# Kernel optimization log

Measured on AMD Instinct MI355X. Metric: run time of the kernel, lower is better.

The kernel has to match this reference:

```python
import jax, jax.numpy as jnp
import numpy as np

RES = 256
XYZ_MIN, XYZ_MAX = -1.0, 1.0
STEPSIZE = 1.0
NEAR, FAR, BG = 0.2, 3.0, 1.0
ALPHA_INIT = 0.01
ACT_SHIFT = float(np.log(1.0 / (1.0 - ALPHA_INIT) - 1.0))
VOXEL = (XYZ_MAX - XYZ_MIN) / RES  # (prod(extent)/R^3)^(1/3) = 2/256
N_SAMPLES = int(np.linalg.norm(np.array([RES + 1] * 3, dtype=np.float64)) / STEPSIZE) + 1  # 446
N_RAYS = 4096
LATENT, NFEAT, RGB_LAT = 64, 32, 15
MULTIRES = 6


def _dense(key, din, dout):
    kw, kb = jax.random.split(key)
    return (jax.random.normal(kw, (din, dout), jnp.float32) / np.float32(np.sqrt(din)),
            jax.random.normal(kb, (dout,), jnp.float32) * 0.01)


def setup_inputs():
    ks = jax.random.split(jax.random.key(0), 16)
    rays_o = jax.random.normal(ks[0], (N_RAYS, 3), jnp.float32) * 1.5
    rays_d = jax.random.normal(ks[1], (N_RAYS, 3), jnp.float32)
    viewdirs = rays_d / jnp.linalg.norm(rays_d, axis=-1, keepdims=True)
    mW1, mb1 = _dense(ks[2], 4, 128)
    mW2, mb2 = _dense(ks[3], 128, 128)
    mW3, mb3 = _dense(ks[4], 128, NFEAT)
    pW1, pb1 = _dense(ks[5], LATENT, 64)
    pW2, pb2 = _dense(ks[6], 64, 64)
    pW3, pb3 = _dense(ks[7], 64, 1 + RGB_LAT)
    emb_dim = 3 + 3 * 2 * MULTIRES  # 39
    dW1, db1 = _dense(ks[8], RGB_LAT + emb_dim, 64)
    dW2, db2 = _dense(ks[9], 64, 64)
    dW3, db3 = _dense(ks[10], 64, 64)
    dW4, db4 = _dense(ks[11], 64, 3)
    return dict(
        rays_o=rays_o, rays_d=rays_d, viewdirs=viewdirs,
        mapping_grid=jax.random.normal(ks[12], (4, RES, RES, RES), jnp.float32) * 0.1,
        feature_vectors=jax.random.normal(ks[13], (NFEAT, LATENT), jnp.float32) * 0.1,
        mW1=mW1, mb1=mb1, mW2=mW2, mb2=mb2, mW3=mW3, mb3=mb3,
        pW1=pW1, pb1=pb1, pW2=pW2, pb2=pb2, pW3=pW3, pb3=pb3,
        dW1=dW1, db1=db1, dW2=dW2, db2=db2, dW3=dW3, db3=db3, dW4=dW4, db4=db4)


def _trilinear(grid, pts):
    # grid: [C,R,R,R]; pts: [...,3] world coords; matches F.grid_sample(align_corners=True)
    # after the flip(-1) in the original (x indexes dim0 of the volume).
    g = jnp.transpose(grid, (1, 2, 3, 0))  # [R,R,R,C]
    u = (pts - XYZ_MIN) / (XYZ_MAX - XYZ_MIN)
    idx = jnp.clip(u * (RES - 1), 0.0, RES - 1.0)
    i0 = jnp.clip(jnp.floor(idx).astype(jnp.int32), 0, RES - 2)
    f = idx - i0.astype(idx.dtype)
    x0, y0, z0 = i0[..., 0], i0[..., 1], i0[..., 2]
    x1, y1, z1 = x0 + 1, y0 + 1, z0 + 1
    fx, fy, fz = f[..., 0:1], f[..., 1:2], f[..., 2:3]
    c000, c001 = g[x0, y0, z0], g[x0, y0, z1]
    c010, c011 = g[x0, y1, z0], g[x0, y1, z1]
    c100, c101 = g[x1, y0, z0], g[x1, y0, z1]
    c110, c111 = g[x1, y1, z0], g[x1, y1, z1]
    c00 = c000 * (1 - fz) + c001 * fz
    c01 = c010 * (1 - fz) + c011 * fz
    c10 = c100 * (1 - fz) + c101 * fz
    c11 = c110 * (1 - fz) + c111 * fz
    c0 = c00 * (1 - fy) + c01 * fy
    c1 = c10 * (1 - fy) + c11 * fy
    return c0 * (1 - fx) + c1 * fx


def _mlp3(x, W1, b1, W2, b2, W3, b3):
    h = jax.nn.relu(x @ W1 + b1)
    h = jax.nn.relu(h @ W2 + b2)
    return h @ W3 + b3


def _dir_embed(v):
    # NeRF positional encoding: [v, sin(2^i v), cos(2^i v)] for i in [0, MULTIRES)
    freqs = 2.0 ** jnp.arange(MULTIRES, dtype=v.dtype)  # [L]
    ang = v[..., None, :] * freqs[:, None]              # [N,L,3]
    sc = jnp.concatenate([jnp.sin(ang), jnp.cos(ang)], axis=-1)  # [N,L,6]
    return jnp.concatenate([v, sc.reshape(v.shape[0], 2 * 3 * MULTIRES)], axis=-1)  # [N,39]


def reference(rays_o, rays_d, viewdirs, mapping_grid, feature_vectors,
              mW1, mb1, mW2, mb2, mW3, mb3,
              pW1, pb1, pW2, pb2, pW3, pb3,
              dW1, db1, dW2, db2, dW3, db3, dW4, db4):
    # --- ray sampling (is_train=False, no jitter) ---
    vec = jnp.where(rays_d == 0, 1e-6, rays_d)
    rate_a = (XYZ_MAX - rays_o) / vec
    rate_b = (XYZ_MIN - rays_o) / vec
    t_min = jnp.clip(jnp.minimum(rate_a, rate_b).max(-1), NEAR, FAR)
    t_max = jnp.clip(jnp.maximum(rate_a, rate_b).min(-1), NEAR, FAR)
    step = STEPSIZE * VOXEL * jnp.arange(N_SAMPLES, dtype=rays_o.dtype)  # [S]
    interpx = t_min[:, None] + step[None, :] / jnp.linalg.norm(rays_d, axis=-1, keepdims=True)
    ray_pts = rays_o[:, None, :] + rays_d[:, None, :] * interpx[..., None]  # [N,S,3]
    valid = ~((t_max <= t_min)[:, None]
              | jnp.any((ray_pts < XYZ_MIN) | (ray_pts > XYZ_MAX), axis=-1))  # [N,S]

    # --- latent extraction: grid sample -> attention over feature bank ---
    mp = _trilinear(mapping_grid, ray_pts)                                  # [N,S,4]
    attn = jax.nn.softmax(_mlp3(mp, mW1, mb1, mW2, mb2, mW3, mb3), axis=-1)  # [N,S,F]
    latent = attn @ feature_vectors                                          # [N,S,latent]

    # --- positional MLP -> density + rgb latent (masked entries zeroed as in torch) ---
    pos = _mlp3(latent, pW1, pb1, pW2, pb2, pW3, pb3)  # [N,S,1+rgb_lat]
    alpha = jnp.where(valid,
                      1.0 - jnp.exp(-jax.nn.softplus(pos[..., 0] + ACT_SHIFT) * STEPSIZE),
                      0.0)
    rgb_latent = jnp.where(valid[..., None], pos[..., 1:], 0.0)

    # --- alpha compositing weights ---
    alphainv_cum = jnp.concatenate(
        [jnp.ones_like(alpha[..., :1]),
         jnp.cumprod(jnp.clip(1.0 - alpha, 1e-10, None), axis=-1)], axis=-1)  # [N,S+1]
    weights = alpha * alphainv_cum[..., :-1]

    # --- directional MLP -> rgb ---
    emb = _dir_embed(viewdirs)                                               # [N,39]
    emb = jnp.broadcast_to(emb[:, None, :], (alpha.shape[0], alpha.shape[1], emb.shape[-1]))
    rgb_feat = jnp.concatenate([rgb_latent, emb], axis=-1)                   # [N,S,54]
    h = jax.nn.relu(rgb_feat @ dW1 + db1)
    h = jax.nn.relu(h @ dW2 + db2)
    h = jax.nn.relu(h @ dW3 + db3)
    raw_rgb = h @ dW4 + db4
    rgb = jnp.where(valid[..., None], jax.nn.sigmoid(raw_rgb[..., :3]), 0.0)

    rgb_marched = jnp.einsum('ns,nsc->nc', weights, rgb) + alphainv_cum[..., -1:] * BG
    return rgb_marched
```

## Files before the change

kernel.cpp:

```cpp
#include <hip/hip_runtime.h>
#include <math.h>

#define ACT_SHIFT -4.5951198501345889f
#define SB 96
#define NSLOTMAX (4096*446)
#define MLP_BLOCKS 1024

typedef _Float16 f16;
typedef f16 f16x8 __attribute__((ext_vector_type(8)));
typedef f16 f16x4 __attribute__((ext_vector_type(4)));
typedef f16 f16x2 __attribute__((ext_vector_type(2)));
typedef float f32x4 __attribute__((ext_vector_type(4)));

#define OFF_CNT  0
#define OFF_RAYI 256
#define OFF_RAYF (OFF_RAYI + 4096*16)
#define OFF_EMBW (OFF_RAYF + 4096*8)
#define OFF_WTS  (OFF_EMBW + 4096*64*4)
#define OFF_SLOT (OFF_WTS + 94208)
#define OFF_WS4H (OFF_SLOT + NSLOTMAX*4)

#define W_MW1 0
#define W_MW2 4096
#define W_MW3 20480
#define W_FV  24576
#define W_P1  26624
#define W_P2  30720
#define W_P3  34816
#define W_D1  35840
#define W_D2  37888
#define W_D3  41984
#define W_D4  46080
#define W_TOT 47104

static __device__ __forceinline__ unsigned short f2h(float x) {
  f16 h = (f16)x; return *(unsigned short*)&h;
}
static __device__ __forceinline__ float h2f(unsigned short u) {
  return (float)(*(f16*)&u);
}

static __device__ __forceinline__ void bar_lds() {
  asm volatile("s_waitcnt lgkmcnt(0)" ::: "memory");
  __builtin_amdgcn_s_barrier();
}

static __device__ __forceinline__ void sample_point(
    float ox, float oy, float oz, float dx, float dy, float dz,
    float tmin, float nrm, int s, float& px, float& py, float& pz) {
  float ix = tmin + (0.0078125f * (float)s) / nrm;
  px = ox + dx * ix; py = oy + dy * ix; pz = oz + dz * ix;
}
static __device__ __forceinline__ int in_box(float px, float py, float pz) {
  return !(px < -1.f || px > 1.f || py < -1.f || py > 1.f ||
           pz < -1.f || pz > 1.f);
}

static __device__ __forceinline__ bool ray_setup(
    const float* rays_o, const float* rays_d, int r,
    float& ox, float& oy, float& oz, float& dx, float& dy, float& dz,
    float& tmin, float& nrm) {
  ox = rays_o[r*3+0]; oy = rays_o[r*3+1]; oz = rays_o[r*3+2];
  dx = rays_d[r*3+0]; dy = rays_d[r*3+1]; dz = rays_d[r*3+2];
  const float vx = (dx == 0.0f) ? 1e-6f : dx;
  const float vy = (dy == 0.0f) ? 1e-6f : dy;
  const float vz = (dz == 0.0f) ? 1e-6f : dz;
  const float rax = ( 1.0f - ox) / vx, rbx = (-1.0f - ox) / vx;
  const float ray_ = ( 1.0f - oy) / vy, rby = (-1.0f - oy) / vy;
  const float raz = ( 1.0f - oz) / vz, rbz = (-1.0f - oz) / vz;
  tmin = fmaxf(fmaxf(fminf(rax,rbx), fminf(ray_,rby)), fminf(raz,rbz));
  tmin = fminf(fmaxf(tmin, 0.2f), 3.0f);
  float tmax = fminf(fminf(fmaxf(rax,rbx), fmaxf(ray_,rby)), fmaxf(raz,rbz));
  tmax = fminf(fmaxf(tmax, 0.2f), 3.0f);
  nrm = sqrtf(dx*dx + dy*dy + dz*dz);
  return tmax <= tmin;
}

extern "C" __global__ void __launch_bounds__(256)
k_setup(const float* __restrict__ rays_o, const float* __restrict__ rays_d,
        int* __restrict__ cnt, int4* __restrict__ rayi,
        float2* __restrict__ rayf) {
  int r = blockIdx.x * 256 + threadIdx.x;
  if (r >= 4096) return;
  float ox,oy,oz,dx,dy,dz,tmin,nrm;
  bool miss = ray_setup(rays_o, rays_d, r, ox,oy,oz,dx,dy,dz, tmin, nrm);
  rayf[r] = make_float2(tmin, nrm);
  if (miss) { rayi[r] = make_int4(0,0,0,0); return; }

  float lo = -1e30f, hi = 1e30f;
  float o3[3] = {ox,oy,oz}, d3[3] = {dx,dy,dz};
#pragma unroll
  for (int c = 0; c < 3; ++c) {
    float o = o3[c], d = d3[c];
    if (d == 0.0f) {
      if (o < -1.f || o > 1.f) { lo = 1e30f; hi = -1e30f; }
    } else {
      float t1 = (-1.f - o) / d, t2 = (1.f - o) / d;
      lo = fmaxf(lo, fminf(t1, t2));
      hi = fminf(hi, fmaxf(t1, t2));
    }
  }
  float k = 0.0078125f / nrm;
  float sf = (lo - tmin) / k - 1.0f;
  float lf = (hi - tmin) / k + 1.0f;
  int first = (int)ceilf (fmaxf(0.f,  fminf(445.f, sf)));
  int last  = (int)floorf(fmaxf(-1.f, fminf(445.f, lf)));
  int n_s = (lf >= sf && last >= first) ? (last - first + 1) : 0;
  int base = 0;
  if (n_s > 0) base = atomicAdd(cnt, n_s);
  rayi[r] = make_int4(base, first, n_s, 0);
}

extern "C" __global__ void __launch_bounds__(64)
k_fill(const int4* __restrict__ rayi, int* __restrict__ slot_map) {
  int r = blockIdx.x;
  int4 ri = rayi[r];
  for (int i = threadIdx.x; i < ri.z; i += 64)
    slot_map[ri.x + i] = (r << 9) | (ri.y + i);
}

extern "C" __global__ void __launch_bounds__(256)
k_embw(const float* __restrict__ viewdirs, const float* __restrict__ dW1,
       const float* __restrict__ db1, float* __restrict__ embW) {
  int idx = blockIdx.x * 256 + threadIdx.x;
  if (idx >= 4096*64) return;
  int ray = idx >> 6, o = idx & 63;
  float v0 = viewdirs[ray*3+0], v1 = viewdirs[ray*3+1], v2 = viewdirs[ray*3+2];
  float acc = db1[o];
  acc = fmaf(v0, dW1[15*64+o], acc);
  acc = fmaf(v1, dW1[16*64+o], acc);
  acc = fmaf(v2, dW1[17*64+o], acc);
#pragma unroll
  for (int fr = 0; fr < 6; ++fr) {
    float f = (float)(1 << fr);
    int rb = 18 + fr*6;
    acc = fmaf(sinf(v0*f), dW1[(rb+0)*64+o], acc);
    acc = fmaf(sinf(v1*f), dW1[(rb+1)*64+o], acc);
    acc = fmaf(sinf(v2*f), dW1[(rb+2)*64+o], acc);
    acc = fmaf(cosf(v0*f), dW1[(rb+3)*64+o], acc);
    acc = fmaf(cosf(v1*f), dW1[(rb+4)*64+o], acc);
    acc = fmaf(cosf(v2*f), dW1[(rb+5)*64+o], acc);
  }
  embW[idx] = acc;
}

extern "C" __global__ void __launch_bounds__(256)
k_pack(const float* __restrict__ mW1, const float* __restrict__ mW2,
       const float* __restrict__ mW3, const float* __restrict__ fv,
       const float* __restrict__ pW1, const float* __restrict__ pW2,
       const float* __restrict__ pW3, const float* __restrict__ dW1,
       const float* __restrict__ dW2, const float* __restrict__ dW3,
       const float* __restrict__ dW4, f16* __restrict__ wts) {
  int i = blockIdx.x * 256 + threadIdx.x;
  if (i >= W_TOT) return;
  float v = 0.f; int l, o, k;
  if (i < W_MW2)        { l=i-W_MW1; o=l>>5; k=l&31;  if (k<4)  v = mW1[k*128+o]; }
  else if (i < W_MW3)   { l=i-W_MW2; o=l>>7; k=l&127; v = mW2[k*128+o]; }
  else if (i < W_FV)    { l=i-W_MW3; o=l>>7; k=l&127; v = mW3[k*32+o]; }
  else if (i < W_P1)    { l=i-W_FV;  o=l>>5; k=l&31;  v = fv[k*64+o]; }
  else if (i < W_P2)    { l=i-W_P1;  o=l>>6; k=l&63;  v = pW1[k*64+o]; }
  else if (i < W_P3)    { l=i-W_P2;  o=l>>6; k=l&63;  v = pW2[k*64+o]; }
  else if (i < W_D1)    { l=i-W_P3;  o=l>>6; k=l&63;  v = pW3[k*16+o]; }
  else if (i < W_D2)    { l=i-W_D1;  o=l>>5; k=l&31;  if (k>=1 && k<16) v = dW1[(k-1)*64+o]; }
  else if (i < W_D3)    { l=i-W_D2;  o=l>>6; k=l&63;  v = dW2[k*64+o]; }
  else if (i < W_D4)    { l=i-W_D3;  o=l>>6; k=l&63;  v = dW3[k*64+o]; }
  else                  { l=i-W_D4;  o=l>>6; k=l&63;  if (o<3)  v = dW4[k*3+o]; }
  wts[i] = (f16)v;
}

template<int KP, int NP, bool RELU, int BMODE, int NW>
__device__ __forceinline__ void layer_mm(
    const f16* __restrict__ Wt, const float* __restrict__ bias,
    const float* __restrict__ embW, const int* sinfo,
    const f16* inb, f16* outb, int wave, int lane,
    int blockbase, unsigned short* ws4h, float& alpha_reg, int& pk_reg) {
  constexpr int ST = SB/16, MT = NP/16, NT = MT*ST, TPW = (NT+NW-1)/NW, KS = KP/32;
  const int c = lane & 15, g = lane >> 4;
  f16x8 Af[KS];
  f32x4 b4 = {0.f,0.f,0.f,0.f};
  int prev_dt = -1;
#pragma unroll
  for (int ti = 0; ti < TPW; ++ti) {
    int t = wave * TPW + ti;
    if (t >= NT) break;
    int dt = t / ST, st = t % ST;
    if (dt != prev_dt) {
      prev_dt = dt;
      const f16* wp = Wt + (size_t)(dt*16 + c) * KP + g*8;
#pragma unroll
      for (int ks = 0; ks < KS; ++ks)
        Af[ks] = *(const f16x8*)(wp + ks*32);
      if (BMODE == 1 || BMODE == 3 || BMODE == 4)
        b4 = *(const f32x4*)(bias + dt*16 + g*4);
    }
    const int row = st*16 + c;
    f32x4 acc = {0.f,0.f,0.f,0.f};
#pragma unroll
    for (int ks = 0; ks < KS; ++ks) {
      int off = (row*256 + (ks*32 + g*8)*2) ^ ((row & 7) << 4);
      f16x8 Bf = *(const f16x8*)((const char*)inb + off);
      acc = __builtin_amdgcn_mfma_f32_16x16x32_f16(Af[ks], Bf, acc, 0, 0, 0);
    }
    if (BMODE == 2) {
      int pk = sinfo[row];
      int ry = (pk < 0) ? 0 : (pk >> 1);
      b4 = *(const f32x4*)(embW + ry*64 + dt*16 + g*4);
    }
    float v0 = acc[0]+b4[0], v1 = acc[1]+b4[1];
    float v2 = acc[2]+b4[2], v3 = acc[3]+b4[3];
    if (BMODE <= 2) {
      if (RELU) {
        v0 = fmaxf(v0,0.f); v1 = fmaxf(v1,0.f);
        v2 = fmaxf(v2,0.f); v3 = fmaxf(v3,0.f);
      }
      f16x4 o = {(f16)v0,(f16)v1,(f16)v2,(f16)v3};
      int off = (row*256 + (dt*16 + g*4)*2) ^ ((row & 7) << 4);
      *(f16x4*)((char*)outb + off) = o;
    } else if (BMODE == 3) {
      pk_reg = sinfo[row];
      if (g == 0) {
        float a = 0.f;
        if (pk_reg >= 0 && (pk_reg & 1)) {
          float x = v0 + ACT_SHIFT;
          float sp = fmaxf(x, 0.f) + log1pf(expf(-fabsf(x)));
          a = 1.f - expf(-sp);
        }
        alpha_reg = a;
        v0 = 0.f;
      }
      f16x4 o = {(f16)v0,(f16)v1,(f16)v2,(f16)v3};
      int off = (row*256 + (g*4)*2) ^ ((row & 7) << 4);
      *(f16x4*)((char*)outb + off) = o;
    } else {
      if (g == 0 && pk_reg >= 0) {
        bool val = (pk_reg & 1) != 0;
        ushort4 u;
        u.x = f2h(alpha_reg);
        u.y = f2h(val ? (1.f/(1.f+expf(-v0))) : 0.f);
        u.z = f2h(val ? (1.f/(1.f+expf(-v1))) : 0.f);
        u.w = f2h(val ? (1.f/(1.f+expf(-v2))) : 0.f);
        *(ushort4*)(ws4h + (size_t)(blockbase + row)*4) = u;
      }
    }
  }
}

struct Pf {
  float v[8];
  float fx, fy, fz;
  int pk;
};

static __device__ __forceinline__ void pf_issue(
    int slot, int total, int c,
    const int* __restrict__ slot_map, const float2* __restrict__ rayf,
    const float* __restrict__ rays_o, const float* __restrict__ rays_d,
    const float* __restrict__ grid, Pf& P) {
  if (slot >= total) {
    P.pk = -2; P.fx = P.fy = P.fz = 0.f;
#pragma unroll
    for (int i = 0; i < 8; ++i) P.v[i] = 0.f;
    return;
  }
  int mi = slot_map[slot];
  int ray = mi >> 9, s = mi & 511;
  float2 tf = rayf[ray];
  float ox = rays_o[ray*3+0], oy = rays_o[ray*3+1], oz = rays_o[ray*3+2];
  float dx = rays_d[ray*3+0], dy = rays_d[ray*3+1], dz = rays_d[ray*3+2];
  float px, py, pz;
  sample_point(ox,oy,oz,dx,dy,dz, tf.x, tf.y, s, px,py,pz);
  P.pk = ray*2 + in_box(px,py,pz);
  float ixf = fminf(fmaxf((px + 1.f) * 0.5f * 255.f, 0.f), 255.f);
  float iyf = fminf(fmaxf((py + 1.f) * 0.5f * 255.f, 0.f), 255.f);
  float izf = fminf(fmaxf((pz + 1.f) * 0.5f * 255.f, 0.f), 255.f);
  int x0 = min((int)ixf, 254), y0 = min((int)iyf, 254), z0 = min((int)izf, 254);
  P.fx = ixf - (float)x0; P.fy = iyf - (float)y0; P.fz = izf - (float)z0;
  const float* gc = grid + (size_t)c * 16777216u;
  int bx0 = x0 << 16, bx1 = bx0 + 65536;
  int by0 = y0 << 8,  by1 = by0 + 256;
  P.v[0] = gc[bx0+by0+z0]; P.v[1] = gc[bx0+by0+z0+1];
  P.v[2] = gc[bx0+by1+z0]; P.v[3] = gc[bx0+by1+z0+1];
  P.v[4] = gc[bx1+by0+z0]; P.v[5] = gc[bx1+by0+z0+1];
  P.v[6] = gc[bx1+by1+z0]; P.v[7] = gc[bx1+by1+z0+1];
}

extern "C" __global__ void __launch_bounds__(512)
k_mlp(const float* __restrict__ rays_o, const float* __restrict__ rays_d,
      const float* __restrict__ grid, const int* __restrict__ slot_map,
      const float2* __restrict__ rayf, const float* __restrict__ embW,
      const f16* __restrict__ wts, const int* __restrict__ cnt,
      const float* __restrict__ mb1, const float* __restrict__ mb2,
      const float* __restrict__ mb3, const float* __restrict__ pb1,
      const float* __restrict__ pb2, const float* __restrict__ pb3,
      const float* __restrict__ db2, const float* __restrict__ db3,
      const float* __restrict__ db4, unsigned short* __restrict__ ws4h) {
  const int total = *cnt;
  const int nch = (total + SB - 1) / SB;
  const int tid = threadIdx.x;
  const int wave = tid >> 6, lane = tid & 63;
  const int sl = tid >> 2, ch = tid & 3;

  __shared__ __align__(16) f16 X[SB*128];
  __shared__ __align__(16) f16 Y[SB*128];
  __shared__ int sinfo[SB];

  Pf P;
  if (tid < SB*4)
    pf_issue(blockIdx.x * SB + sl, total, ch, slot_map, rayf, rays_o, rays_d,
             grid, P);

  for (int chunk = blockIdx.x; chunk < nch; chunk += gridDim.x) {
    const int blockbase = chunk * SB;
    float alpha_reg = 0.f; int pk_reg = -2;

    if (tid < SB*4) {
      float c00 = P.v[0]*(1.f-P.fz) + P.v[1]*P.fz;
      float c01 = P.v[2]*(1.f-P.fz) + P.v[3]*P.fz;
      float c10 = P.v[4]*(1.f-P.fz) + P.v[5]*P.fz;
      float c11 = P.v[6]*(1.f-P.fz) + P.v[7]*P.fz;
      float c0v = c00*(1.f-P.fy) + c01*P.fy;
      float c1v = c10*(1.f-P.fy) + c11*P.fy;
      float mv  = c0v*(1.f-P.fx) + c1v*P.fx;
      if (ch == 0) sinfo[sl] = P.pk;
      int off = (sl*256 + ch*2) ^ ((sl & 7) << 4);
      *(f16*)((char*)X + off) = (f16)mv;
    }
    for (int idx = tid; idx < SB*14; idx += 512) {
      int row = idx / 14, dim = 4 + (idx % 14)*2;
      int off = (row*256 + dim*2) ^ ((row & 7) << 4);
      f16x2 z = {(f16)0.f, (f16)0.f};
      *(f16x2*)((char*)X + off) = z;
    }
    if (tid < SB*4)
      pf_issue((chunk + gridDim.x) * SB + sl, total, ch, slot_map, rayf,
               rays_o, rays_d, grid, P);
    bar_lds();

    layer_mm<32,128,true,1,8>(wts+W_MW1, mb1, nullptr, sinfo, X, Y, wave, lane, blockbase, ws4h, alpha_reg, pk_reg);
    bar_lds();
    layer_mm<128,128,true,1,8>(wts+W_MW2, mb2, nullptr, sinfo, Y, X, wave, lane, blockbase, ws4h, alpha_reg, pk_reg);
    bar_lds();
    layer_mm<128,32,false,1,8>(wts+W_MW3, mb3, nullptr, sinfo, X, Y, wave, lane, blockbase, ws4h, alpha_reg, pk_reg);
    bar_lds();

    if (tid < SB) {
      int row = tid;
      float v[32];
#pragma unroll
      for (int p = 0; p < 16; ++p) {
        int off = (row*256 + p*4) ^ ((row & 7) << 4);
        f16x2 two = *(const f16x2*)((const char*)Y + off);
        v[2*p] = (float)two[0]; v[2*p+1] = (float)two[1];
      }
      float m = -1e30f;
#pragma unroll
      for (int i = 0; i < 32; ++i) m = fmaxf(m, v[i]);
      float sum = 0.f;
#pragma unroll
      for (int i = 0; i < 32; ++i) { v[i] = expf(v[i] - m); sum += v[i]; }
      float inv = 1.f / sum;
#pragma unroll
      for (int p = 0; p < 16; ++p) {
        int off = (row*256 + p*4) ^ ((row & 7) << 4);
        f16x2 two = {(f16)(v[2*p]*inv), (f16)(v[2*p+1]*inv)};
        *(f16x2*)((char*)Y + off) = two;
      }
    }
    bar_lds();

    layer_mm<32,64,false,0,8>(wts+W_FV, nullptr, nullptr, sinfo, Y, X, wave, lane, blockbase, ws4h, alpha_reg, pk_reg);
    bar_lds();
    layer_mm<64,64,true,1,8>(wts+W_P1, pb1, nullptr, sinfo, X, Y, wave, lane, blockbase, ws4h, alpha_reg, pk_reg);
    bar_lds();
    layer_mm<64,64,true,1,8>(wts+W_P2, pb2, nullptr, sinfo, Y, X, wave, lane, blockbase, ws4h, alpha_reg, pk_reg);
    bar_lds();
    layer_mm<64,16,false,3,8>(wts+W_P3, pb3, nullptr, sinfo, X, Y, wave, lane, blockbase, ws4h, alpha_reg, pk_reg);
    bar_lds();
    layer_mm<32,64,true,2,8>(wts+W_D1, nullptr, embW, sinfo, Y, X, wave, lane, blockbase, ws4h, alpha_reg, pk_reg);
    bar_lds();
    layer_mm<64,64,true,1,8>(wts+W_D2, db2, nullptr, sinfo, X, Y, wave, lane, blockbase, ws4h, alpha_reg, pk_reg);
    bar_lds();
    layer_mm<64,64,true,1,8>(wts+W_D3, db3, nullptr, sinfo, Y, X, wave, lane, blockbase, ws4h, alpha_reg, pk_reg);
    bar_lds();
    layer_mm<64,16,false,4,8>(wts+W_D4, db4, nullptr, sinfo, X, Y, wave, lane, blockbase, ws4h, alpha_reg, pk_reg);
    bar_lds();
  }
}

extern "C" __global__ void __launch_bounds__(256)
k_scan(const ushort4* __restrict__ ws4h, const int4* __restrict__ rayi,
       float* __restrict__ out) {
  const int wid = (blockIdx.x * 256 + threadIdx.x) >> 6;
  const int ln  = threadIdx.x & 63;
  if (wid >= 4096) return;
  int4 ri = rayi[wid];
  int base = ri.x, n_s = ri.z;

  float T = 1.0f, ar = 0.f, ag = 0.f, ab = 0.f;
  int nc = (n_s + 63) >> 6;
  for (int cck = 0; cck < nc; ++cck) {
    int j = cck*64 + ln;
    float a = 0.f, rr = 0.f, gg = 0.f, bb = 0.f;
    if (j < n_s) {
      ushort4 u = ws4h[(size_t)base + j];
      a = h2f(u.x); rr = h2f(u.y); gg = h2f(u.z); bb = h2f(u.w);
    }
    float p = fmaxf(1.0f - a, 1e-10f);
#pragma unroll
    for (int off = 1; off < 64; off <<= 1) {
      float o = __shfl_up(p, off);
      if (ln >= off) p *= o;
    }
    float pe = __shfl_up(p, 1);
    if (ln == 0) pe = 1.0f;
    float wgt = a * T * pe;
    ar = fmaf(wgt, rr, ar);
    ag = fmaf(wgt, gg, ag);
    ab = fmaf(wgt, bb, ab);
    T *= __shfl(p, 63);
  }
#pragma unroll
  for (int off = 32; off; off >>= 1) {
    ar += __shfl_down(ar, off);
    ag += __shfl_down(ag, off);
    ab += __shfl_down(ab, off);
  }
  if (ln == 0) {
    out[wid*3+0] = ar + T;
    out[wid*3+1] = ag + T;
    out[wid*3+2] = ab + T;
  }
}

extern "C" void kernel_launch(void* const* d_in, const int* in_sizes, int n_in,
                              void* d_out, int out_size, void* d_ws, size_t ws_size,
                              hipStream_t stream) {
  const float* rays_o   = (const float*)d_in[0];
  const float* rays_d   = (const float*)d_in[1];
  const float* viewdirs = (const float*)d_in[2];
  const float* grid     = (const float*)d_in[3];
  const float* fv       = (const float*)d_in[4];
  const float* mW1 = (const float*)d_in[5];  const float* mb1 = (const float*)d_in[6];
  const float* mW2 = (const float*)d_in[7];  const float* mb2 = (const float*)d_in[8];
  const float* mW3 = (const float*)d_in[9];  const float* mb3 = (const float*)d_in[10];
  const float* pW1 = (const float*)d_in[11]; const float* pb1 = (const float*)d_in[12];
  const float* pW2 = (const float*)d_in[13]; const float* pb2 = (const float*)d_in[14];
  const float* pW3 = (const float*)d_in[15]; const float* pb3 = (const float*)d_in[16];
  const float* dW1 = (const float*)d_in[17]; const float* db1 = (const float*)d_in[18];
  const float* dW2 = (const float*)d_in[19]; const float* db2 = (const float*)d_in[20];
  const float* dW3 = (const float*)d_in[21]; const float* db3 = (const float*)d_in[22];
  const float* dW4 = (const float*)d_in[23]; const float* db4 = (const float*)d_in[24];
  float* out = (float*)d_out;

  char* ws = (char*)d_ws;
  int*     cnt      = (int*)(ws + OFF_CNT);
  int4*    rayi     = (int4*)(ws + OFF_RAYI);
  float2*  rayf     = (float2*)(ws + OFF_RAYF);
  float*   embW     = (float*)(ws + OFF_EMBW);
  f16*     wts      = (f16*)(ws + OFF_WTS);
  int*     slot_map = (int*)(ws + OFF_SLOT);
  unsigned short* ws4h = (unsigned short*)(ws + OFF_WS4H);

  hipMemsetAsync(cnt, 0, 4, stream);
  k_setup<<<16, 256, 0, stream>>>(rays_o, rays_d, cnt, rayi, rayf);
  k_fill<<<4096, 64, 0, stream>>>(rayi, slot_map);
  k_embw<<<1024, 256, 0, stream>>>(viewdirs, dW1, db1, embW);
  k_pack<<<(W_TOT+255)/256, 256, 0, stream>>>(mW1, mW2, mW3, fv, pW1, pW2, pW3,
                                              dW1, dW2, dW3, dW4, wts);
  k_mlp<<<MLP_BLOCKS, 512, 0, stream>>>(rays_o, rays_d, grid, slot_map, rayf,
                                        embW, wts, cnt, mb1, mb2, mb3,
                                        pb1, pb2, pb3, db2, db3, db4, ws4h);
  k_scan<<<1024, 256, 0, stream>>>((const ushort4*)ws4h, rayi, out);
}
```

Before: 105.4 us.

## Switch MLP to 32x32 MFMA with register-resident weights and dynamic chunk queue

Rewrites the fused MLP kernel to use 32x32x16 MFMA tiles on 128-sample chunks, keeping most layer weights resident in registers across chunks instead of reloading them per tile. Chunks are handed out through an atomic work queue with 256 persistent blocks rather than a fixed grid stride. The softmax is computed in registers straight from the MFMA accumulators. The fill, embedding and weight-pack kernels are merged into one auxiliary launch, and biases are packed into a padded buffer. The intent is to cut weight reload traffic, per-tile overhead and launch count, at the cost of much higher register pressure and lower occupancy.

```diff
diff --git a/kernel.cpp b/kernel.cpp
--- a/kernel.cpp
+++ b/kernel.cpp
@@ -2,36 +2,36 @@
 #include <math.h>
 
 #define ACT_SHIFT -4.5951198501345889f
-#define SB 96
+#define SB 128
 #define NSLOTMAX (4096*446)
-#define MLP_BLOCKS 1024
 
 typedef _Float16 f16;
 typedef f16 f16x8 __attribute__((ext_vector_type(8)));
 typedef f16 f16x4 __attribute__((ext_vector_type(4)));
-typedef f16 f16x2 __attribute__((ext_vector_type(2)));
 typedef float f32x4 __attribute__((ext_vector_type(4)));
+typedef float f32x16 __attribute__((ext_vector_type(16)));
 
 #define OFF_CNT  0
 #define OFF_RAYI 256
 #define OFF_RAYF (OFF_RAYI + 4096*16)
 #define OFF_EMBW (OFF_RAYF + 4096*8)
 #define OFF_WTS  (OFF_EMBW + 4096*64*4)
-#define OFF_SLOT (OFF_WTS + 94208)
+#define OFF_BIAS (OFF_WTS + 92160)
+#define OFF_SLOT (OFF_BIAS + 8192)
 #define OFF_WS4H (OFF_SLOT + NSLOTMAX*4)
 
 #define W_MW1 0
-#define W_MW2 4096
-#define W_MW3 20480
-#define W_FV  24576
-#define W_P1  26624
-#define W_P2  30720
-#define W_P3  34816
-#define W_D1  35840
-#define W_D2  37888
-#define W_D3  41984
-#define W_D4  46080
-#define W_TOT 47104
+#define W_MW2 2048
+#define W_MW3 18432
+#define W_FV  22528
+#define W_P1  24576
+#define W_P2  28672
+#define W_P3  32768
+#define W_D1  34816
+#define W_D2  35840
+#define W_D3  39936
+#define W_D4  44032
+#define W_TOT 46080
 
 static __device__ __forceinline__ unsigned short f2h(float x) {
   f16 h = (f16)x; return *(unsigned short*)&h;
@@ -111,137 +111,132 @@
   rayi[r] = make_int4(base, first, n_s, 0);
 }
 
-extern "C" __global__ void __launch_bounds__(64)
-k_fill(const int4* __restrict__ rayi, int* __restrict__ slot_map) {
-  int r = blockIdx.x;
-  int4 ri = rayi[r];
-  for (int i = threadIdx.x; i < ri.z; i += 64)
-    slot_map[ri.x + i] = (r << 9) | (ri.y + i);
-}
-
 extern "C" __global__ void __launch_bounds__(256)
-k_embw(const float* __restrict__ viewdirs, const float* __restrict__ dW1,
-       const float* __restrict__ db1, float* __restrict__ embW) {
-  int idx = blockIdx.x * 256 + threadIdx.x;
-  if (idx >= 4096*64) return;
-  int ray = idx >> 6, o = idx & 63;
-  float v0 = viewdirs[ray*3+0], v1 = viewdirs[ray*3+1], v2 = viewdirs[ray*3+2];
-  float acc = db1[o];
-  acc = fmaf(v0, dW1[15*64+o], acc);
-  acc = fmaf(v1, dW1[16*64+o], acc);
-  acc = fmaf(v2, dW1[17*64+o], acc);
-#pragma unroll
-  for (int fr = 0; fr < 6; ++fr) {
-    float f = (float)(1 << fr);
-    int rb = 18 + fr*6;
-    acc = fmaf(sinf(v0*f), dW1[(rb+0)*64+o], acc);
-    acc = fmaf(sinf(v1*f), dW1[(rb+1)*64+o], acc);
-    acc = fmaf(sinf(v2*f), dW1[(rb+2)*64+o], acc);
-    acc = fmaf(cosf(v0*f), dW1[(rb+3)*64+o], acc);
-    acc = fmaf(cosf(v1*f), dW1[(rb+4)*64+o], acc);
-    acc = fmaf(cosf(v2*f), dW1[(rb+5)*64+o], acc);
-  }
-  embW[idx] = acc;
-}
-
-extern "C" __global__ void __launch_bounds__(256)
-k_pack(const float* __restrict__ mW1, const float* __restrict__ mW2,
-       const float* __restrict__ mW3, const float* __restrict__ fv,
-       const float* __restrict__ pW1, const float* __restrict__ pW2,
-       const float* __restrict__ pW3, const float* __restrict__ dW1,
-       const float* __restrict__ dW2, const float* __restrict__ dW3,
-       const float* __restrict__ dW4, f16* __restrict__ wts) {
-  int i = blockIdx.x * 256 + threadIdx.x;
-  if (i >= W_TOT) return;
-  float v = 0.f; int l, o, k;
-  if (i < W_MW2)        { l=i-W_MW1; o=l>>5; k=l&31;  if (k<4)  v = mW1[k*128+o]; }
-  else if (i < W_MW3)   { l=i-W_MW2; o=l>>7; k=l&127; v = mW2[k*128+o]; }
-  else if (i < W_FV)    { l=i-W_MW3; o=l>>7; k=l&127; v = mW3[k*32+o]; }
-  else if (i < W_P1)    { l=i-W_FV;  o=l>>5; k=l&31;  v = fv[k*64+o]; }
-  else if (i < W_P2)    { l=i-W_P1;  o=l>>6; k=l&63;  v = pW1[k*64+o]; }
-  else if (i < W_P3)    { l=i-W_P2;  o=l>>6; k=l&63;  v = pW2[k*64+o]; }
-  else if (i < W_D1)    { l=i-W_P3;  o=l>>6; k=l&63;  v = pW3[k*16+o]; }
-  else if (i < W_D2)    { l=i-W_D1;  o=l>>5; k=l&31;  if (k>=1 && k<16) v = dW1[(k-1)*64+o]; }
-  else if (i < W_D3)    { l=i-W_D2;  o=l>>6; k=l&63;  v = dW2[k*64+o]; }
-  else if (i < W_D4)    { l=i-W_D3;  o=l>>6; k=l&63;  v = dW3[k*64+o]; }
-  else                  { l=i-W_D4;  o=l>>6; k=l&63;  if (o<3)  v = dW4[k*3+o]; }
-  wts[i] = (f16)v;
-}
-
-template<int KP, int NP, bool RELU, int BMODE, int NW>
-__device__ __forceinline__ void layer_mm(
-    const f16* __restrict__ Wt, const float* __restrict__ bias,
-    const float* __restrict__ embW, const int* sinfo,
-    const f16* inb, f16* outb, int wave, int lane,
-    int blockbase, unsigned short* ws4h, float& alpha_reg, int& pk_reg) {
-  constexpr int ST = SB/16, MT = NP/16, NT = MT*ST, TPW = (NT+NW-1)/NW, KS = KP/32;
-  const int c = lane & 15, g = lane >> 4;
-  f16x8 Af[KS];
-  f32x4 b4 = {0.f,0.f,0.f,0.f};
-  int prev_dt = -1;
-#pragma unroll
-  for (int ti = 0; ti < TPW; ++ti) {
-    int t = wave * TPW + ti;
-    if (t >= NT) break;
-    int dt = t / ST, st = t % ST;
-    if (dt != prev_dt) {
-      prev_dt = dt;
-      const f16* wp = Wt + (size_t)(dt*16 + c) * KP + g*8;
-#pragma unroll
-      for (int ks = 0; ks < KS; ++ks)
-        Af[ks] = *(const f16x8*)(wp + ks*32);
-      if (BMODE == 1 || BMODE == 3 || BMODE == 4)
-        b4 = *(const f32x4*)(bias + dt*16 + g*4);
-    }
-    const int row = st*16 + c;
-    f32x4 acc = {0.f,0.f,0.f,0.f};
-#pragma unroll
-    for (int ks = 0; ks < KS; ++ks) {
-      int off = (row*256 + (ks*32 + g*8)*2) ^ ((row & 7) << 4);
-      f16x8 Bf = *(const f16x8*)((const char*)inb + off);
-      acc = __builtin_amdgcn_mfma_f32_16x16x32_f16(Af[ks], Bf, acc, 0, 0, 0);
-    }
-    if (BMODE == 2) {
-      int pk = sinfo[row];
-      int ry = (pk < 0) ? 0 : (pk >> 1);
-      b4 = *(const f32x4*)(embW + ry*64 + dt*16 + g*4);
-    }
-    float v0 = acc[0]+b4[0], v1 = acc[1]+b4[1];
-    float v2 = acc[2]+b4[2], v3 = acc[3]+b4[3];
-    if (BMODE <= 2) {
-      if (RELU) {
-        v0 = fmaxf(v0,0.f); v1 = fmaxf(v1,0.f);
-        v2 = fmaxf(v2,0.f); v3 = fmaxf(v3,0.f);
-      }
-      f16x4 o = {(f16)v0,(f16)v1,(f16)v2,(f16)v3};
-      int off = (row*256 + (dt*16 + g*4)*2) ^ ((row & 7) << 4);
-      *(f16x4*)((char*)outb + off) = o;
-    } else if (BMODE == 3) {
-      pk_reg = sinfo[row];
-      if (g == 0) {
-        float a = 0.f;
-        if (pk_reg >= 0 && (pk_reg & 1)) {
-          float x = v0 + ACT_SHIFT;
-          float sp = fmaxf(x, 0.f) + log1pf(expf(-fabsf(x)));
-          a = 1.f - expf(-sp);
-        }
-        alpha_reg = a;
-        v0 = 0.f;
-      }
-      f16x4 o = {(f16)v0,(f16)v1,(f16)v2,(f16)v3};
-      int off = (row*256 + (g*4)*2) ^ ((row & 7) << 4);
-      *(f16x4*)((char*)outb + off) = o;
-    } else {
-      if (g == 0 && pk_reg >= 0) {
-        bool val = (pk_reg & 1) != 0;
-        ushort4 u;
-        u.x = f2h(alpha_reg);
-        u.y = f2h(val ? (1.f/(1.f+expf(-v0))) : 0.f);
-        u.z = f2h(val ? (1.f/(1.f+expf(-v1))) : 0.f);
-        u.w = f2h(val ? (1.f/(1.f+expf(-v2))) : 0.f);
-        *(ushort4*)(ws4h + (size_t)(blockbase + row)*4) = u;
-      }
-    }
+k_aux(const float* __restrict__ viewdirs, const int4* __restrict__ rayi,
+      int* __restrict__ slot_map,
+      const float* __restrict__ mW1, const float* __restrict__ mW2,
+      const float* __restrict__ mW3, const float* __restrict__ fv,
+      const float* __restrict__ pW1, const float* __restrict__ pW2,
+      const float* __restrict__ pW3, const float* __restrict__ dW1,
+      const float* __restrict__ dW2, const float* __restrict__ dW3,
+      const float* __restrict__ dW4,
+      const float* __restrict__ mb1, const float* __restrict__ mb2,
+      const float* __restrict__ mb3, const float* __restrict__ pb1,
+      const float* __restrict__ pb2, const float* __restrict__ pb3,
+      const float* __restrict__ db1, const float* __restrict__ db2,
+      const float* __restrict__ db3, const float* __restrict__ db4,
+      f16* __restrict__ wts, float* __restrict__ bias,
+      float* __restrict__ embW) {
+  const int b = blockIdx.x, t = threadIdx.x;
+  if (b < 1024) {
+    int idx = b * 256 + t;
+    int ray = idx >> 6, o = idx & 63;
+    float v0 = viewdirs[ray*3+0], v1 = viewdirs[ray*3+1], v2 = viewdirs[ray*3+2];
+    float acc = db1[o];
+    acc = fmaf(v0, dW1[15*64+o], acc);
+    acc = fmaf(v1, dW1[16*64+o], acc);
+    acc = fmaf(v2, dW1[17*64+o], acc);
+#pragma unroll
+    for (int fr = 0; fr < 6; ++fr) {
+      float f = (float)(1 << fr);
+      int rb = 18 + fr*6;
+      acc = fmaf(sinf(v0*f), dW1[(rb+0)*64+o], acc);
+      acc = fmaf(sinf(v1*f), dW1[(rb+1)*64+o], acc);
+      acc = fmaf(sinf(v2*f), dW1[(rb+2)*64+o], acc);
+      acc = fmaf(cosf(v0*f), dW1[(rb+3)*64+o], acc);
+      acc = fmaf(cosf(v1*f), dW1[(rb+4)*64+o], acc);
+      acc = fmaf(cosf(v2*f), dW1[(rb+5)*64+o], acc);
+    }
+    embW[idx] = acc;
+  } else if (b < 1280) {
+    int ray = (b - 1024) * 16 + (t >> 4);
+    int4 ri = rayi[ray];
+    for (int i = t & 15; i < ri.z; i += 16)
+      slot_map[ri.x + i] = (ray << 9) | (ri.y + i);
+  } else if (b < 1460) {
+    int i = (b - 1280) * 256 + t;
+    if (i >= W_TOT) return;
+    float v = 0.f; int l, o, k;
+    if (i < W_MW2)      { l=i;        o=l>>4; k=l&15;  if (k<4)  v = mW1[k*128+o]; }
+    else if (i < W_MW3) { l=i-W_MW2;  o=l>>7; k=l&127; v = mW2[k*128+o]; }
+    else if (i < W_FV)  { l=i-W_MW3;  o=l>>7; k=l&127; v = mW3[k*32+o]; }
+    else if (i < W_P1)  { l=i-W_FV;   o=l>>5; k=l&31;  v = fv[k*64+o]; }
+    else if (i < W_P2)  { l=i-W_P1;   o=l>>6; k=l&63;  v = pW1[k*64+o]; }
+    else if (i < W_P3)  { l=i-W_P2;   o=l>>6; k=l&63;  v = pW2[k*64+o]; }
+    else if (i < W_D1)  { l=i-W_P3;   o=l>>6; k=l&63;  if (o<16) v = pW3[k*16+o]; }
+    else if (i < W_D2)  { l=i-W_D1;   o=l>>4; k=l&15;  if (k>=1) v = dW1[(k-1)*64+o]; }
+    else if (i < W_D3)  { l=i-W_D2;   o=l>>6; k=l&63;  v = dW2[k*64+o]; }
+    else if (i < W_D4)  { l=i-W_D3;   o=l>>6; k=l&63;  v = dW3[k*64+o]; }
+    else                { l=i-W_D4;   o=l>>6; k=l&63;  if (o<3)  v = dW4[k*3+o]; }
+    wts[i] = (f16)v;
+  } else {
+    int i = (b - 1460) * 256 + t;
+    if (i >= 1408) return;
+    int L = i >> 7, o = i & 127;
+    float v = 0.f;
+    if      (L == 0)            v = mb1[o];
+    else if (L == 1)            v = mb2[o];
+    else if (L == 2 && o < 32)  v = mb3[o];
+    else if (L == 4 && o < 64)  v = pb1[o];
+    else if (L == 5 && o < 64)  v = pb2[o];
+    else if (L == 6 && o < 16)  v = pb3[o];
+    else if (L == 8 && o < 64)  v = db2[o];
+    else if (L == 9 && o < 64)  v = db3[o];
+    else if (L == 10 && o < 3)  v = db4[o];
+    bias[i] = v;
+  }
+}
+
+template<int KS>
+static __device__ __forceinline__ void load_b(const f16* Xb, int st, int lane,
+                                              f16x8* B) {
+  const int r = st*32 + (lane & 31);
+  const int base = r*256 + ((lane >> 5) * 16);
+#pragma unroll
+  for (int ks = 0; ks < KS; ++ks) {
+    int off = (base + ks*32) ^ ((r & 15) << 4);
+    B[ks] = *(const f16x8*)((const char*)Xb + off);
+  }
+}
+
+template<int KS>
+static __device__ __forceinline__ void load_a(const f16* __restrict__ wbase,
+                                              int dt, int lane, f16x8* A) {
+  const f16* wp = wbase + (size_t)(dt*32 + (lane & 31)) * (KS*16) + (lane >> 5) * 8;
+#pragma unroll
+  for (int ks = 0; ks < KS; ++ks) A[ks] = *(const f16x8*)(wp + ks*16);
+}
+
+template<int KS>
+static __device__ __forceinline__ f32x16 mm(const f16x8* A, const f16x8* B) {
+  f32x16 acc;
+#pragma unroll
+  for (int i = 0; i < 16; ++i) acc[i] = 0.f;
+#pragma unroll
+  for (int ks = 0; ks < KS; ++ks)
+    acc = __builtin_amdgcn_mfma_f32_32x32x16_f16(A[ks], B[ks], acc, 0, 0, 0);
+  return acc;
+}
+
+template<bool RELU, int NQ>
+static __device__ __forceinline__ void store_c(f16* Yb, int st, int dtb, int lane,
+                                               const f32x16& acc,
+                                               const float* __restrict__ bp) {
+  const int r = st*32 + (lane & 31);
+  const int gp = (lane >> 5) * 4;
+#pragma unroll
+  for (int q = 0; q < NQ; ++q) {
+    const int db = dtb + q*8 + gp;
+    f32x4 b4 = *(const f32x4*)(bp + db);
+    float v0 = acc[4*q+0]+b4[0], v1 = acc[4*q+1]+b4[1];
+    float v2 = acc[4*q+2]+b4[2], v3 = acc[4*q+3]+b4[3];
+    if (RELU) {
+      v0 = fmaxf(v0,0.f); v1 = fmaxf(v1,0.f);
+      v2 = fmaxf(v2,0.f); v3 = fmaxf(v3,0.f);
+    }
+    f16x4 o = {(f16)v0,(f16)v1,(f16)v2,(f16)v3};
+    int off = (r*256 + db*2) ^ ((r & 15) << 4);
+    *(f16x4*)((char*)Yb + off) = o;
   }
 }
 
@@ -288,32 +283,50 @@
 k_mlp(const float* __restrict__ rays_o, const float* __restrict__ rays_d,
       const float* __restrict__ grid, const int* __restrict__ slot_map,
       const float2* __restrict__ rayf, const float* __restrict__ embW,
-      const f16* __restrict__ wts, const int* __restrict__ cnt,
-      const float* __restrict__ mb1, const float* __restrict__ mb2,
-      const float* __restrict__ mb3, const float* __restrict__ pb1,
-      const float* __restrict__ pb2, const float* __restrict__ pb3,
-      const float* __restrict__ db2, const float* __restrict__ db3,
-      const float* __restrict__ db4, unsigned short* __restrict__ ws4h) {
-  const int total = *cnt;
-  const int nch = (total + SB - 1) / SB;
+      const f16* __restrict__ wts, const float* __restrict__ bias,
+      int* __restrict__ cnt, unsigned short* __restrict__ ws4h) {
+  const int total = cnt[0];
+  const int nch = (total + 127) >> 7;
+  int* qh = cnt + 1;
   const int tid = threadIdx.x;
-  const int wave = tid >> 6, lane = tid & 63;
+  const int wv = tid >> 6, lane = tid & 63;
   const int sl = tid >> 2, ch = tid & 3;
+  const int dthi = wv >> 2;
+  const int stw = wv & 3;
 
   __shared__ __align__(16) f16 X[SB*128];
   __shared__ __align__(16) f16 Y[SB*128];
   __shared__ int sinfo[SB];
+  __shared__ int q_next;
+
+  f16x8 aMW1a[1], aMW1b[1], aFV[2], aP1[4], aP2[4], aD1[1], aD2[4], aD3[4];
+  load_a<1>(wts+W_MW1, dthi,   lane, aMW1a);
+  load_a<1>(wts+W_MW1, dthi+2, lane, aMW1b);
+  load_a<2>(wts+W_FV,  dthi,   lane, aFV);
+  load_a<4>(wts+W_P1,  dthi,   lane, aP1);
+  load_a<4>(wts+W_P2,  dthi,   lane, aP2);
+  load_a<1>(wts+W_D1,  dthi,   lane, aD1);
+  load_a<4>(wts+W_D2,  dthi,   lane, aD2);
+  load_a<4>(wts+W_D3,  dthi,   lane, aD3);
+  f16x8 aP3[4], aD4[4];
+  if (wv < 4) {
+    load_a<4>(wts+W_P3, 0, lane, aP3);
+    load_a<4>(wts+W_D4, 0, lane, aD4);
+  }
+
+  if (tid == 0) q_next = atomicAdd(qh, 1);
+  __syncthreads();
+  int cur = q_next;
 
   Pf P;
-  if (tid < SB*4)
-    pf_issue(blockIdx.x * SB + sl, total, ch, slot_map, rayf, rays_o, rays_d,
-             grid, P);
-
-  for (int chunk = blockIdx.x; chunk < nch; chunk += gridDim.x) {
-    const int blockbase = chunk * SB;
-    float alpha_reg = 0.f; int pk_reg = -2;
-
-    if (tid < SB*4) {
+  pf_issue((cur < nch) ? cur*128 + sl : total, total, ch,
+           slot_map, rayf, rays_o, rays_d, grid, P);
+
+  while (cur < nch) {
+    const int blockbase = cur << 7;
+    if (tid == 0) q_next = atomicAdd(qh, 1);
+
+    {
       float c00 = P.v[0]*(1.f-P.fz) + P.v[1]*P.fz;
       float c01 = P.v[2]*(1.f-P.fz) + P.v[3]*P.fz;
       float c10 = P.v[4]*(1.f-P.fz) + P.v[5]*P.fz;
@@ -322,68 +335,134 @@
       float c1v = c10*(1.f-P.fy) + c11*P.fy;
       float mv  = c0v*(1.f-P.fx) + c1v*P.fx;
       if (ch == 0) sinfo[sl] = P.pk;
-      int off = (sl*256 + ch*2) ^ ((sl & 7) << 4);
+      int off = (sl*256 + ch*2) ^ ((sl & 15) << 4);
       *(f16*)((char*)X + off) = (f16)mv;
-    }
-    for (int idx = tid; idx < SB*14; idx += 512) {
-      int row = idx / 14, dim = 4 + (idx % 14)*2;
-      int off = (row*256 + dim*2) ^ ((row & 7) << 4);
-      f16x2 z = {(f16)0.f, (f16)0.f};
-      *(f16x2*)((char*)X + off) = z;
-    }
-    if (tid < SB*4)
-      pf_issue((chunk + gridDim.x) * SB + sl, total, ch, slot_map, rayf,
-               rays_o, rays_d, grid, P);
+      if (ch < 3) {
+        int zo = (sl*256 + 8 + ch*8) ^ ((sl & 15) << 4);
+        *(unsigned long long*)((char*)X + zo) = 0ull;
+      }
+    }
     bar_lds();
-
-    layer_mm<32,128,true,1,8>(wts+W_MW1, mb1, nullptr, sinfo, X, Y, wave, lane, blockbase, ws4h, alpha_reg, pk_reg);
+    const int nxt = q_next;
+    pf_issue((nxt < nch) ? nxt*128 + sl : total, total, ch,
+             slot_map, rayf, rays_o, rays_d, grid, P);
+
+    float alpha_reg = 0.f; int pk_reg = -2;
+
+    { f16x8 B[1]; load_b<1>(X, stw, lane, B);
+      f32x16 a0 = mm<1>(aMW1a, B);
+      store_c<true,4>(Y, stw, dthi*32, lane, a0, bias + 0*128);
+      f32x16 a1 = mm<1>(aMW1b, B);
+      store_c<true,4>(Y, stw, (dthi+2)*32, lane, a1, bias + 0*128);
+    } bar_lds();
+
+    { f16x8 B[8]; load_b<8>(Y, stw, lane, B);
+      f16x8 A8[8];
+      load_a<8>(wts+W_MW2, dthi, lane, A8);
+      f32x16 a0 = mm<8>(A8, B);
+      store_c<true,4>(X, stw, dthi*32, lane, a0, bias + 1*128);
+      load_a<8>(wts+W_MW2, dthi+2, lane, A8);
+      f32x16 a1 = mm<8>(A8, B);
+      store_c<true,4>(X, stw, (dthi+2)*32, lane, a1, bias + 1*128);
+    } bar_lds();
+
+    if (wv < 4) {
+      f16x8 B[8]; load_b<8>(X, wv, lane, B);
+      f16x8 A8[8]; load_a<8>(wts+W_MW3, 0, lane, A8);
+      f32x16 acc = mm<8>(A8, B);
+      const int gp = (lane >> 5) * 4;
+      float v[16];
+#pragma unroll
+      for (int q = 0; q < 4; ++q) {
+        f32x4 b4 = *(const f32x4*)(bias + 2*128 + q*8 + gp);
+#pragma unroll
+        for (int i = 0; i < 4; ++i) v[4*q+i] = acc[4*q+i] + b4[i];
+      }
+      float mx = v[0];
+#pragma unroll
+      for (int i = 1; i < 16; ++i) mx = fmaxf(mx, v[i]);
+      mx = fmaxf(mx, __shfl_xor(mx, 32));
+      float s = 0.f;
+#pragma unroll
+      for (int i = 0; i < 16; ++i) { v[i] = expf(v[i] - mx); s += v[i]; }
+      s += __shfl_xor(s, 32);
+      float inv = 1.f / s;
+      const int r = wv*32 + (lane & 31);
+#pragma unroll
+      for (int q = 0; q < 4; ++q) {
+        const int db = q*8 + gp;
+        f16x4 o = {(f16)(v[4*q+0]*inv), (f16)(v[4*q+1]*inv),
+                   (f16)(v[4*q+2]*inv), (f16)(v[4*q+3]*inv)};
+        int off = (r*256 + db*2) ^ ((r & 15) << 4);
+        *(f16x4*)((char*)Y + off) = o;
+      }
+    }
     bar_lds();
-    layer_mm<128,128,true,1,8>(wts+W_MW2, mb2, nullptr, sinfo, Y, X, wave, lane, blockbase, ws4h, alpha_reg, pk_reg);
+
+    { f16x8 B[2]; load_b<2>(Y, stw, lane, B);
+      f32x16 a0 = mm<2>(aFV, B);
+      store_c<false,4>(X, stw, dthi*32, lane, a0, bias + 3*128);
+    } bar_lds();
+
+    { f16x8 B[4]; load_b<4>(X, stw, lane, B);
+      f32x16 a0 = mm<4>(aP1, B);
+      store_c<true,4>(Y, stw, dthi*32, lane, a0, bias + 4*128);
+    } bar_lds();
+
+    { f16x8 B[4]; load_b<4>(Y, stw, lane, B);
+      f32x16 a0 = mm<4>(aP2, B);
+      store_c<true,4>(X, stw, dthi*32, lane, a0, bias + 5*128);
+    } bar_lds();
+
+    if (wv < 4) {
+      f16x8 B[4]; load_b<4>(X, wv, lane, B);
+      f32x16 acc = mm<4>(aP3, B);
+      pk_reg = sinfo[wv*32 + (lane & 31)];
+      if (lane < 32) {
+        alpha_reg = 0.f;
+        if (pk_reg >= 0 && (pk_reg & 1)) {
+          float x = acc[0] + bias[6*128 + 0] + ACT_SHIFT;
+          float sp = fmaxf(x, 0.f) + log1pf(expf(-fabsf(x)));
+          alpha_reg = 1.f - expf(-sp);
+        }
+      }
+      store_c<false,2>(Y, wv, 0, lane, acc, bias + 6*128);
+    }
     bar_lds();
-    layer_mm<128,32,false,1,8>(wts+W_MW3, mb3, nullptr, sinfo, X, Y, wave, lane, blockbase, ws4h, alpha_reg, pk_reg);
+
+    { f16x8 B[1]; load_b<1>(Y, stw, lane, B);
+      f32x16 acc = mm<1>(aD1, B);
+      int pkc = sinfo[stw*32 + (lane & 31)];
+      int ry = (pkc < 0) ? 0 : (pkc >> 1);
+      store_c<true,4>(X, stw, dthi*32, lane, acc, embW + (size_t)ry*64);
+    } bar_lds();
+
+    { f16x8 B[4]; load_b<4>(X, stw, lane, B);
+      f32x16 a0 = mm<4>(aD2, B);
+      store_c<true,4>(Y, stw, dthi*32, lane, a0, bias + 8*128);
+    } bar_lds();
+
+    { f16x8 B[4]; load_b<4>(Y, stw, lane, B);
+      f32x16 a0 = mm<4>(aD3, B);
+      store_c<true,4>(X, stw, dthi*32, lane, a0, bias + 9*128);
+    } bar_lds();
+
+    if (wv < 4) {
+      f16x8 B[4]; load_b<4>(X, wv, lane, B);
+      f32x16 acc = mm<4>(aD4, B);
+      if (lane < 32 && pk_reg >= 0) {
+        const float* bp = bias + 10*128;
+        bool val = (pk_reg & 1) != 0;
+        ushort4 u;
+        u.x = f2h(alpha_reg);
+        u.y = f2h(val ? 1.f/(1.f+expf(-(acc[0]+bp[0]))) : 0.f);
+        u.z = f2h(val ? 1.f/(1.f+expf(-(acc[1]+bp[1]))) : 0.f);
+        u.w = f2h(val ? 1.f/(1.f+expf(-(acc[2]+bp[2]))) : 0.f);
+        *(ushort4*)(ws4h + (size_t)(blockbase + wv*32 + (lane & 31))*4) = u;
+      }
+    }
     bar_lds();
-
-    if (tid < SB) {
-      int row = tid;
-      float v[32];
-#pragma unroll
-      for (int p = 0; p < 16; ++p) {
-        int off = (row*256 + p*4) ^ ((row & 7) << 4);
-        f16x2 two = *(const f16x2*)((const char*)Y + off);
-        v[2*p] = (float)two[0]; v[2*p+1] = (float)two[1];
-      }
-      float m = -1e30f;
-#pragma unroll
-      for (int i = 0; i < 32; ++i) m = fmaxf(m, v[i]);
-      float sum = 0.f;
-#pragma unroll
-      for (int i = 0; i < 32; ++i) { v[i] = expf(v[i] - m); sum += v[i]; }
-      float inv = 1.f / sum;
-#pragma unroll
-      for (int p = 0; p < 16; ++p) {
-        int off = (row*256 + p*4) ^ ((row & 7) << 4);
-        f16x2 two = {(f16)(v[2*p]*inv), (f16)(v[2*p+1]*inv)};
-        *(f16x2*)((char*)Y + off) = two;
-      }
-    }
-    bar_lds();
-
-    layer_mm<32,64,false,0,8>(wts+W_FV, nullptr, nullptr, sinfo, Y, X, wave, lane, blockbase, ws4h, alpha_reg, pk_reg);
-    bar_lds();
-    layer_mm<64,64,true,1,8>(wts+W_P1, pb1, nullptr, sinfo, X, Y, wave, lane, blockbase, ws4h, alpha_reg, pk_reg);
-    bar_lds();
-    layer_mm<64,64,true,1,8>(wts+W_P2, pb2, nullptr, sinfo, Y, X, wave, lane, blockbase, ws4h, alpha_reg, pk_reg);
-    bar_lds();
-    layer_mm<64,16,false,3,8>(wts+W_P3, pb3, nullptr, sinfo, X, Y, wave, lane, blockbase, ws4h, alpha_reg, pk_reg);
-    bar_lds();
-    layer_mm<32,64,true,2,8>(wts+W_D1, nullptr, embW, sinfo, Y, X, wave, lane, blockbase, ws4h, alpha_reg, pk_reg);
-    bar_lds();
-    layer_mm<64,64,true,1,8>(wts+W_D2, db2, nullptr, sinfo, X, Y, wave, lane, blockbase, ws4h, alpha_reg, pk_reg);
-    bar_lds();
-    layer_mm<64,64,true,1,8>(wts+W_D3, db3, nullptr, sinfo, Y, X, wave, lane, blockbase, ws4h, alpha_reg, pk_reg);
-    bar_lds();
-    layer_mm<64,16,false,4,8>(wts+W_D4, db4, nullptr, sinfo, X, Y, wave, lane, blockbase, ws4h, alpha_reg, pk_reg);
-    bar_lds();
+    cur = nxt;
   }
 }
 
@@ -458,17 +537,18 @@
   float2*  rayf     = (float2*)(ws + OFF_RAYF);
   float*   embW     = (float*)(ws + OFF_EMBW);
   f16*     wts      = (f16*)(ws + OFF_WTS);
+  float*   bias     = (float*)(ws + OFF_BIAS);
   int*     slot_map = (int*)(ws + OFF_SLOT);
   unsigned short* ws4h = (unsigned short*)(ws + OFF_WS4H);
 
-  hipMemsetAsync(cnt, 0, 4, stream);
+  hipMemsetAsync(cnt, 0, 8, stream);
   k_setup<<<16, 256, 0, stream>>>(rays_o, rays_d, cnt, rayi, rayf);
-  k_fill<<<4096, 64, 0, stream>>>(rayi, slot_map);
-  k_embw<<<1024, 256, 0, stream>>>(viewdirs, dW1, db1, embW);
-  k_pack<<<(W_TOT+255)/256, 256, 0, stream>>>(mW1, mW2, mW3, fv, pW1, pW2, pW3,
-                                              dW1, dW2, dW3, dW4, wts);
-  k_mlp<<<MLP_BLOCKS, 512, 0, stream>>>(rays_o, rays_d, grid, slot_map, rayf,
-                                        embW, wts, cnt, mb1, mb2, mb3,
-                                        pb1, pb2, pb3, db2, db3, db4, ws4h);
+  k_aux<<<1466, 256, 0, stream>>>(viewdirs, rayi, slot_map,
+                                  mW1, mW2, mW3, fv, pW1, pW2, pW3,
+                                  dW1, dW2, dW3, dW4,
+                                  mb1, mb2, mb3, pb1, pb2, pb3,
+                                  db1, db2, db3, db4, wts, bias, embW);
+  k_mlp<<<256, 512, 0, stream>>>(rays_o, rays_d, grid, slot_map, rayf,
+                                 embW, wts, bias, cnt, ws4h);
   k_scan<<<1024, 256, 0, stream>>>((const ushort4*)ws4h, rayi, out);
 }
```

Result: faster. 103.2 us (-2.0%).
